# Performance work log

Hardware: AMD Instinct MI355X
Metric: run time of the kernel (lower is better)

Reference implementation:

```python
import jax, jax.numpy as jnp
import numpy as np

DIM = 1024
CTX_DIM = 768
H = 16


def setup_inputs() -> dict:
    key = jax.random.key(0)
    k1, k2, k3, k4, k5 = jax.random.split(key, 5)
    x = jax.random.normal(k1, (2, 2048, DIM), dtype=jnp.float32)
    context = jax.random.normal(k2, (2, 2048, CTX_DIM), dtype=jnp.float32)
    # Linear weights stored as [in, out] (y = x @ W); no biases per module.
    s = 0.02
    Wq = jax.random.normal(k3, (DIM, DIM), dtype=jnp.float32) * s
    Wkv = jax.random.normal(k4, (CTX_DIM, 2 * DIM), dtype=jnp.float32) * s
    Wo = jax.random.normal(k5, (DIM, DIM), dtype=jnp.float32) * s
    return {"x": x, "context": context, "Wq": Wq, "Wkv": Wkv, "Wo": Wo}


def reference(x, context, Wq, Wkv, Wo):
    B, N, C = x.shape
    Dh = C // H  # head dim
    scale = Dh ** -0.5
    M = context.shape[1]
    q = (x @ Wq).reshape(B, N, H, Dh).transpose(0, 2, 1, 3)      # [B,H,N,Dh]
    kv = context @ Wkv                                            # [B,M,2C]
    k, v = jnp.split(kv, 2, axis=-1)
    k = k.reshape(B, M, H, Dh).transpose(0, 2, 1, 3)              # [B,H,M,Dh]
    v = v.reshape(B, M, H, Dh).transpose(0, 2, 1, 3)              # [B,H,M,Dh]
    attn = jax.nn.softmax(jnp.einsum('bhnd,bhmd->bhnm', q, k) * scale, axis=-1)
    out = jnp.einsum('bhnm,bhmd->bhnd', attn, v)                  # [B,H,N,Dh]
    out = out.transpose(0, 2, 1, 3).reshape(B, N, C)
    return out @ Wo  # dropout is identity in eval / p=0
```

## Files before the change

### kernel.cpp

```cpp
#include <hip/hip_runtime.h>

typedef __attribute__((ext_vector_type(4))) float f32x4;
typedef __attribute__((ext_vector_type(8))) short short8;
typedef __attribute__((ext_vector_type(4))) unsigned int u32x4;
typedef unsigned short u16;
typedef unsigned int u32;
typedef unsigned long long u64;

__device__ __forceinline__ u16 f2bf(float f) {
  u32 u = __builtin_bit_cast(u32, f);
  u += 0x7fffu + ((u >> 16) & 1u);
  return (u16)(u >> 16);
}
__device__ __forceinline__ u16 f2bf_t(float f) {
  return (u16)(__builtin_bit_cast(u32, f) >> 16);
}

__device__ __forceinline__ void gl2lds16(const u16* g, const u16* l) {
  __builtin_amdgcn_global_load_lds(
      (const __attribute__((address_space(1))) u32*)g,
      (__attribute__((address_space(3))) u32*)(u32)(u64)l,
      16, 0, 0);
}

__device__ __forceinline__ void cast_body(const float* __restrict__ s,
                                          u16* __restrict__ d, int blk,
                                          int tid) {
  long i = (long)blk * 256 + tid;
  const f32x4* sp = (const f32x4*)(s + i * 8);
  f32x4 a = sp[0], b = sp[1];
  u16 t[8];
#pragma unroll
  for (int j = 0; j < 4; j++) {
    t[j] = f2bf(a[j]);
    t[4 + j] = f2bf(b[j]);
  }
  *(u32x4*)(d + i * 8) = *(u32x4*)t;
}

__device__ __forceinline__ void transpose_body(const float* __restrict__ W,
                                               u16* __restrict__ WT, int K,
                                               int N, int k0, int n0, int tid,
                                               u16* T) {
#pragma unroll
  for (int i = 0; i < 4; i++) {
    int c = tid + 256 * i;
    int row = c >> 4;
    int ch = c & 15;
    f32x4 f = *(const f32x4*)(W + (long)(k0 + row) * N + n0 + ch * 4);
#pragma unroll
    for (int j = 0; j < 4; j++) T[(ch * 4 + j) * 72 + row] = f2bf(f[j]);
  }
  __syncthreads();
#pragma unroll
  for (int i = 0; i < 2; i++) {
    int c = tid + 256 * i;
    int row = c >> 3;
    int ch = c & 7;
    u32x4 v = *(u32x4*)&T[row * 72 + ch * 8];
    *(u32x4*)(WT + (long)(n0 + row) * K + k0 + ch * 8) = v;
  }
}

__global__ __launch_bounds__(256) void prep(
    const float* __restrict__ x, const float* __restrict__ ctx,
    const float* __restrict__ Wq, const float* __restrict__ Wkv,
    const float* __restrict__ Wo, u16* __restrict__ xb,
    u16* __restrict__ ctxb, u16* __restrict__ wqT, u16* __restrict__ wkvT,
    u16* __restrict__ woT) {
  __shared__ __align__(16) u16 T[64 * 72];
  const int b = blockIdx.x, tid = threadIdx.x;
  if (b < 2048) {
    cast_body(x, xb, b, tid);
  } else if (b < 3584) {
    cast_body(ctx, ctxb, b - 2048, tid);
  } else if (b < 3840) {
    int idx = b - 3584;
    transpose_body(Wq, wqT, 1024, 1024, (idx >> 4) * 64, (idx & 15) * 64, tid, T);
  } else if (b < 4224) {
    int idx = b - 3840;
    transpose_body(Wkv, wkvT, 768, 2048, (idx >> 5) * 64, (idx & 31) * 64, tid, T);
  } else {
    int idx = b - 4224;
    transpose_body(Wo, woT, 1024, 1024, (idx >> 4) * 64, (idx & 15) * 64, tid, T);
  }
}

__device__ __forceinline__ void gemm128_core(
    const u16* __restrict__ A, const u16* __restrict__ Bt, int Kstride,
    int Klen, long brow, long bcol, int tid, u16* As, u16* Bs,
    f32x4 (&acc)[4][4]) {
  const int lane = tid & 63, wv = tid >> 6;
  const int l15 = lane & 15, quad = lane >> 4;
  const int wr = (wv >> 1) * 64, wc = (wv & 1) * 64;
  const int sr = lane >> 3, sc = lane & 7;
  const int csw = ((sc ^ sr) & 7) * 8;

  const u16* ag[4];
  const u16* bg[4];
  const u16* al[4];
  const u16* bl[4];
#pragma unroll
  for (int n = 0; n < 4; n++) {
    int row = wv * 32 + n * 8;
    ag[n] = A + (brow + row + sr) * (long)Kstride + csw;
    al[n] = &As[row * 64];
    bg[n] = Bt + (bcol + row + sr) * (long)Kstride + csw;
    bl[n] = &Bs[row * 64];
  }

  for (int kt = 0; kt < Klen; kt += 64) {
    __syncthreads();
#pragma unroll
    for (int n = 0; n < 4; n++) gl2lds16(ag[n] + kt, al[n]);
#pragma unroll
    for (int n = 0; n < 4; n++) gl2lds16(bg[n] + kt, bl[n]);
    __syncthreads();
#pragma unroll
    for (int kk = 0; kk < 2; kk++) {
      short8 af[4], bf[4];
#pragma unroll
      for (int i = 0; i < 4; i++) {
        int row = wr + i * 16 + l15;
        af[i] = *(short8*)&As[row * 64 + (((kk * 4 + quad) ^ (row & 7)) << 3)];
      }
#pragma unroll
      for (int j = 0; j < 4; j++) {
        int row = wc + j * 16 + l15;
        bf[j] = *(short8*)&Bs[row * 64 + (((kk * 4 + quad) ^ (row & 7)) << 3)];
      }
#pragma unroll
      for (int i = 0; i < 4; i++)
#pragma unroll
        for (int j = 0; j < 4; j++)
          acc[i][j] = __builtin_amdgcn_mfma_f32_16x16x32_bf16(
              af[i], bf[j], acc[i][j], 0, 0, 0);
    }
  }
}

__global__ __launch_bounds__(256, 3) void fused_qkv(
    const u16* __restrict__ xb, const u16* __restrict__ ctxb,
    const u16* __restrict__ wqT, const u16* __restrict__ wkvT,
    u16* __restrict__ Qb, u16* __restrict__ Kfrag, u16* __restrict__ Vfrag,
    float qscale) {
  __shared__ __align__(16) u16 As[128 * 64];
  __shared__ __align__(16) u16 Bs[128 * 64];
  const int tid = threadIdx.x;
  const int lane = tid & 63, wv = tid >> 6;
  const int l15 = lane & 15, quad = lane >> 4;
  const int wr = (wv >> 1) * 64, wc = (wv & 1) * 64;

  f32x4 acc[4][4];
#pragma unroll
  for (int i = 0; i < 4; i++)
#pragma unroll
    for (int j = 0; j < 4; j++) acc[i][j] = (f32x4){0.f, 0.f, 0.f, 0.f};

  int bid = blockIdx.x;
  if (bid < 256) {
    long brow = (long)(bid >> 3) * 128, bcol = (long)(bid & 7) * 128;
    gemm128_core(xb, wqT, 1024, 1024, brow, bcol, tid, As, Bs, acc);
#pragma unroll
    for (int i = 0; i < 4; i++)
#pragma unroll
      for (int j = 0; j < 4; j++)
#pragma unroll
        for (int r = 0; r < 4; r++) {
          long row = brow + wr + i * 16 + quad * 4 + r;
          long col = bcol + wc + j * 16 + l15;
          Qb[row * 1024 + col] = f2bf(acc[i][j][r] * qscale);
        }
    return;
  }

  bid -= 256;
  long brow = (long)(bid >> 4) * 128, bcol = (long)(bid & 15) * 128;
  gemm128_core(ctxb, wkvT, 768, 768, brow, bcol, tid, As, Bs, acc);

  const bool is_k = (bcol < 1024);
  __syncthreads();
#pragma unroll
  for (int round = 0; round < 2; round++) {
    if ((wv >> 1) == round) {
      if (is_k) {
#pragma unroll
        for (int i = 0; i < 4; i++)
#pragma unroll
          for (int j = 0; j < 4; j++) {
            int d = j * 16 + l15;
            int off = (wv & 1) * 4096 + ((d >> 5) * 4 + i) * 512 +
                      (((d >> 3) & 3) * 16 + quad * 4) * 8 + (d & 7);
#pragma unroll
            for (int r = 0; r < 4; r++) As[off + r * 8] = f2bf(acc[i][j][r]);
          }
      } else {
#pragma unroll
        for (int i = 0; i < 4; i++)
#pragma unroll
          for (int j = 0; j < 4; j++) {
            int off = (wv & 1) * 4096 + ((i >> 1) * 4 + j) * 512 +
                      (quad * 16 + l15) * 8 + (i & 1) * 4;
            u16 t4[4];
#pragma unroll
            for (int r = 0; r < 4; r++) t4[r] = f2bf(acc[i][j][r]);
            *(u64*)&As[off] = *(const u64*)t4;
          }
      }
    }
    __syncthreads();
    long mg = brow + round * 64;
    int b_ = (int)(mg >> 11), mt = (int)((mg >> 6) & 31);
#pragma unroll
    for (int h2 = 0; h2 < 2; h2++) {
      int h = (int)((is_k ? bcol : bcol - 1024) >> 6) + h2;
      u16* dst = (is_k ? Kfrag : Vfrag) + ((long)(b_ * 16 + h) * 32 + mt) * 4096;
#pragma unroll
      for (int p = 0; p < 2; p++) {
        int c = p * 256 + tid;
        *(u32x4*)(dst + c * 8) = *(u32x4*)&As[h2 * 4096 + c * 8];
      }
    }
    __syncthreads();
  }
}

__global__ __launch_bounds__(256, 3) void gemm_o(
    const u16* __restrict__ A, const u16* __restrict__ Bt,
    float* __restrict__ C) {
  __shared__ __align__(16) u16 As[128 * 64];
  __shared__ __align__(16) u16 Bs[128 * 64];
  const int tid = threadIdx.x;
  const int lane = tid & 63, wv = tid >> 6;
  const int l15 = lane & 15, quad = lane >> 4;
  const int wr = (wv >> 1) * 64, wc = (wv & 1) * 64;
  long brow = (long)blockIdx.y * 128, bcol = (long)blockIdx.x * 128;

  f32x4 acc[4][4];
#pragma unroll
  for (int i = 0; i < 4; i++)
#pragma unroll
    for (int j = 0; j < 4; j++) acc[i][j] = (f32x4){0.f, 0.f, 0.f, 0.f};

  gemm128_core(A, Bt, 1024, 1024, brow, bcol, tid, As, Bs, acc);

#pragma unroll
  for (int i = 0; i < 4; i++)
#pragma unroll
    for (int j = 0; j < 4; j++)
#pragma unroll
      for (int r = 0; r < 4; r++) {
        long row = brow + wr + i * 16 + quad * 4 + r;
        long col = bcol + wc + j * 16 + l15;
        C[row * 1024 + col] = acc[i][j][r];
      }
}

__global__ __launch_bounds__(256, 2) void attn_kernel(
    const u16* __restrict__ Q, const u16* __restrict__ Kfrag,
    const u16* __restrict__ Vfrag, u16* __restrict__ AO) {
  const int tid = threadIdx.x;
  const int lane = tid & 63, wave = tid >> 6;
  const int l15 = lane & 15, quad = lane >> 4;
  const int bh = blockIdx.y;
  const int b = bh >> 4, h = bh & 15;
  const long qrow0 = (long)b * 2048 + blockIdx.x * 128;

  short8 qf[2][2];
#pragma unroll
  for (int qt = 0; qt < 2; qt++)
#pragma unroll
    for (int kk = 0; kk < 2; kk++)
      qf[qt][kk] = *(const short8*)&Q[(qrow0 + wave * 32 + qt * 16 + l15) * 1024 +
                                      h * 64 + kk * 32 + quad * 8];

  f32x4 O[2][5];
#pragma unroll
  for (int qt = 0; qt < 2; qt++)
#pragma unroll
    for (int dt = 0; dt < 5; dt++) O[qt][dt] = (f32x4){0.f, 0.f, 0.f, 0.f};

  u32x4 ones_u = {0x3F803F80u, 0x3F803F80u, 0x3F803F80u, 0x3F803F80u};
  short8 ones = __builtin_bit_cast(short8, ones_u);

  const u16* kbase = Kfrag + (long)bh * 32 * 4096 + lane * 8;
  const u16* vbase = Vfrag + (long)bh * 32 * 4096 + lane * 8;

  auto load_k = [&](short8(&kf)[2][4], int tile) {
    const u16* kt = kbase + (long)tile * 4096;
#pragma unroll
    for (int kk = 0; kk < 2; kk++)
#pragma unroll
      for (int t = 0; t < 4; t++)
        kf[kk][t] = *(const short8*)(kt + (kk * 4 + t) * 512);
  };

  auto step = [&](short8(&kc)[2][4], short8(&kn)[2][4], int tile) {
    short8 vf[2][4];
    const u16* vt = vbase + (long)tile * 4096;
#pragma unroll
    for (int kk = 0; kk < 2; kk++)
#pragma unroll
      for (int dt = 0; dt < 4; dt++)
        vf[kk][dt] = *(const short8*)(vt + (kk * 4 + dt) * 512);
    if (tile + 1 < 32) load_k(kn, tile + 1);

    f32x4 s[4][2];
#pragma unroll
    for (int m4 = 0; m4 < 4; m4++)
#pragma unroll
      for (int qt = 0; qt < 2; qt++) s[m4][qt] = (f32x4){0.f, 0.f, 0.f, 0.f};
#pragma unroll
    for (int kk = 0; kk < 2; kk++)
#pragma unroll
      for (int m4 = 0; m4 < 4; m4++)
#pragma unroll
        for (int qt = 0; qt < 2; qt++)
          s[m4][qt] = __builtin_amdgcn_mfma_f32_16x16x32_bf16(
              kc[kk][m4], qf[qt][kk], s[m4][qt], 0, 0, 0);

#pragma unroll
    for (int kk = 0; kk < 2; kk++) {
#pragma unroll
      for (int qt = 0; qt < 2; qt++) {
        u32 w[4];
#pragma unroll
        for (int half = 0; half < 2; half++) {
          f32x4 sv = s[2 * kk + half][qt];
          u32 lo = (u32)f2bf_t(__builtin_amdgcn_exp2f(sv[0] - 24.f)) |
                   ((u32)f2bf_t(__builtin_amdgcn_exp2f(sv[1] - 24.f)) << 16);
          u32 hi = (u32)f2bf_t(__builtin_amdgcn_exp2f(sv[2] - 24.f)) |
                   ((u32)f2bf_t(__builtin_amdgcn_exp2f(sv[3] - 24.f)) << 16);
          w[half * 2] = lo;
          w[half * 2 + 1] = hi;
        }
        short8 pa = __builtin_bit_cast(short8, *(u32x4*)w);
#pragma unroll
        for (int dt = 0; dt < 4; dt++)
          O[qt][dt] = __builtin_amdgcn_mfma_f32_16x16x32_bf16(
              pa, vf[kk][dt], O[qt][dt], 0, 0, 0);
        O[qt][4] = __builtin_amdgcn_mfma_f32_16x16x32_bf16(
            pa, ones, O[qt][4], 0, 0, 0);
      }
    }
  };

  short8 ka[2][4], kb2[2][4];
  load_k(ka, 0);
  for (int tile = 0; tile < 32; tile += 2) {
    step(ka, kb2, tile);
    step(kb2, ka, tile + 1);
  }

#pragma unroll
  for (int qt = 0; qt < 2; qt++) {
    float inv[4];
#pragma unroll
    for (int r = 0; r < 4; r++) inv[r] = 1.f / O[qt][4][r];
#pragma unroll
    for (int dt = 0; dt < 4; dt++)
#pragma unroll
      for (int r = 0; r < 4; r++) {
        long row = qrow0 + wave * 32 + qt * 16 + quad * 4 + r;
        int col = h * 64 + dt * 16 + l15;
        AO[row * 1024 + col] = f2bf(O[qt][dt][r] * inv[r]);
      }
  }
}

extern "C" void kernel_launch(void* const* d_in, const int* in_sizes, int n_in,
                              void* d_out, int out_size, void* d_ws,
                              size_t ws_size, hipStream_t stream) {
  const float* x = (const float*)d_in[0];
  const float* ctx = (const float*)d_in[1];
  const float* Wq = (const float*)d_in[2];
  const float* Wkv = (const float*)d_in[3];
  const float* Wo = (const float*)d_in[4];
  float* out = (float*)d_out;

  u16* ws = (u16*)d_ws;
  u16* wqT = ws;
  u16* wkvT = wqT + 1048576;
  u16* woT = wkvT + 1572864;
  u16* Qb = woT + 1048576;
  u16* Kfrag = Qb + 4194304;
  u16* Vfrag = Kfrag + 4194304;
  u16* xb = Vfrag + 4194304;
  u16* ctxb = xb + 4194304;
  u16* AOb = xb;

  const float qscale = 0.125f * 1.4426950408889634f;

  prep<<<dim3(4480), 256, 0, stream>>>(x, ctx, Wq, Wkv, Wo, xb, ctxb, wqT,
                                       wkvT, woT);

  fused_qkv<<<dim3(768), 256, 0, stream>>>(xb, ctxb, wqT, wkvT, Qb, Kfrag,
                                           Vfrag, qscale);

  attn_kernel<<<dim3(16, 32), 256, 0, stream>>>(Qb, Kfrag, Vfrag, AOb);

  gemm_o<<<dim3(8, 32), 256, 0, stream>>>(AOb, woT, out);
}
```

Baseline: 191.2 us.

## Stage K/V tiles in LDS and split key range across two wave halves

The attention kernel now uses 512 threads per block. K/V fragments are staged into double-buffered shared memory with global_load_lds, so the four query-chunk waves share one copy instead of each wave reading them from global memory separately. The key sequence is split between two groups of four waves, and their partial outputs and row sums are combined through LDS at the end. This reduces global K/V traffic and register pressure, at the cost of block-wide barriers every tile and a final reduction step.

```diff
diff --git a/kernel.cpp b/kernel.cpp
--- a/kernel.cpp
+++ b/kernel.cpp
@@ -256,22 +256,24 @@
       }
 }
 
-__global__ __launch_bounds__(256, 2) void attn_kernel(
+__global__ __launch_bounds__(512, 4) void attn_kernel(
     const u16* __restrict__ Q, const u16* __restrict__ Kfrag,
     const u16* __restrict__ Vfrag, u16* __restrict__ AO) {
+  __shared__ __align__(16) u16 smem[2][4][4096];
   const int tid = threadIdx.x;
-  const int lane = tid & 63, wave = tid >> 6;
+  const int lane = tid & 63, wv = tid >> 6;
+  const int qc = wv & 3, half = wv >> 2;
   const int l15 = lane & 15, quad = lane >> 4;
   const int bh = blockIdx.y;
   const int b = bh >> 4, h = bh & 15;
-  const long qrow0 = (long)b * 2048 + blockIdx.x * 128;
+  const long qrow0 = (long)b * 2048 + blockIdx.x * 128 + qc * 32;
 
   short8 qf[2][2];
 #pragma unroll
   for (int qt = 0; qt < 2; qt++)
 #pragma unroll
     for (int kk = 0; kk < 2; kk++)
-      qf[qt][kk] = *(const short8*)&Q[(qrow0 + wave * 32 + qt * 16 + l15) * 1024 +
+      qf[qt][kk] = *(const short8*)&Q[(qrow0 + qt * 16 + l15) * 1024 +
                                       h * 64 + kk * 32 + quad * 8];
 
   f32x4 O[2][5];
@@ -283,88 +285,109 @@
   u32x4 ones_u = {0x3F803F80u, 0x3F803F80u, 0x3F803F80u, 0x3F803F80u};
   short8 ones = __builtin_bit_cast(short8, ones_u);
 
-  const u16* kbase = Kfrag + (long)bh * 32 * 4096 + lane * 8;
-  const u16* vbase = Vfrag + (long)bh * 32 * 4096 + lane * 8;
-
-  auto load_k = [&](short8(&kf)[2][4], int tile) {
-    const u16* kt = kbase + (long)tile * 4096;
-#pragma unroll
-    for (int kk = 0; kk < 2; kk++)
+  const u16* kg0 = Kfrag + (long)bh * 32 * 4096;
+  const u16* vg0 = Vfrag + (long)bh * 32 * 4096;
+  const int so = wv * 512 + lane * 8;
+
+  auto stage = [&](int nb, int i) {
+    const u16* k0 = kg0 + (long)i * 4096 + so;
+    const u16* v0 = vg0 + (long)i * 4096 + so;
+    gl2lds16(k0, &smem[nb][0][wv * 512]);
+    gl2lds16(v0, &smem[nb][1][wv * 512]);
+    gl2lds16(k0 + 16 * 4096, &smem[nb][2][wv * 512]);
+    gl2lds16(v0 + 16 * 4096, &smem[nb][3][wv * 512]);
+  };
+
+  stage(0, 0);
+  __syncthreads();
+
+  for (int i = 0; i < 16; i++) {
+    const int cur = i & 1;
+    if (i < 15) stage(cur ^ 1, i + 1);
+
+    const u16* Ks = &smem[cur][half * 2][0] + lane * 8;
+    const u16* Vs = &smem[cur][half * 2 + 1][0] + lane * 8;
+
+    f32x4 s[4][2];
+#pragma unroll
+    for (int m4 = 0; m4 < 4; m4++)
+#pragma unroll
+      for (int qt = 0; qt < 2; qt++) s[m4][qt] = (f32x4){0.f, 0.f, 0.f, 0.f};
+#pragma unroll
+    for (int kk = 0; kk < 2; kk++) {
+      short8 kf[4];
 #pragma unroll
       for (int t = 0; t < 4; t++)
-        kf[kk][t] = *(const short8*)(kt + (kk * 4 + t) * 512);
-  };
-
-  auto step = [&](short8(&kc)[2][4], short8(&kn)[2][4], int tile) {
-    short8 vf[2][4];
-    const u16* vt = vbase + (long)tile * 4096;
-#pragma unroll
-    for (int kk = 0; kk < 2; kk++)
-#pragma unroll
-      for (int dt = 0; dt < 4; dt++)
-        vf[kk][dt] = *(const short8*)(vt + (kk * 4 + dt) * 512);
-    if (tile + 1 < 32) load_k(kn, tile + 1);
-
-    f32x4 s[4][2];
-#pragma unroll
-    for (int m4 = 0; m4 < 4; m4++)
-#pragma unroll
-      for (int qt = 0; qt < 2; qt++) s[m4][qt] = (f32x4){0.f, 0.f, 0.f, 0.f};
-#pragma unroll
-    for (int kk = 0; kk < 2; kk++)
+        kf[t] = *(const short8*)(Ks + (kk * 4 + t) * 512);
 #pragma unroll
       for (int m4 = 0; m4 < 4; m4++)
 #pragma unroll
         for (int qt = 0; qt < 2; qt++)
           s[m4][qt] = __builtin_amdgcn_mfma_f32_16x16x32_bf16(
-              kc[kk][m4], qf[qt][kk], s[m4][qt], 0, 0, 0);
+              kf[m4], qf[qt][kk], s[m4][qt], 0, 0, 0);
+    }
 
 #pragma unroll
     for (int kk = 0; kk < 2; kk++) {
+      short8 vf[4];
+#pragma unroll
+      for (int dt = 0; dt < 4; dt++)
+        vf[dt] = *(const short8*)(Vs + (kk * 4 + dt) * 512);
 #pragma unroll
       for (int qt = 0; qt < 2; qt++) {
         u32 w[4];
 #pragma unroll
-        for (int half = 0; half < 2; half++) {
-          f32x4 sv = s[2 * kk + half][qt];
+        for (int hw = 0; hw < 2; hw++) {
+          f32x4 sv = s[2 * kk + hw][qt];
           u32 lo = (u32)f2bf_t(__builtin_amdgcn_exp2f(sv[0] - 24.f)) |
                    ((u32)f2bf_t(__builtin_amdgcn_exp2f(sv[1] - 24.f)) << 16);
           u32 hi = (u32)f2bf_t(__builtin_amdgcn_exp2f(sv[2] - 24.f)) |
                    ((u32)f2bf_t(__builtin_amdgcn_exp2f(sv[3] - 24.f)) << 16);
-          w[half * 2] = lo;
-          w[half * 2 + 1] = hi;
+          w[hw * 2] = lo;
+          w[hw * 2 + 1] = hi;
         }
         short8 pa = __builtin_bit_cast(short8, *(u32x4*)w);
 #pragma unroll
         for (int dt = 0; dt < 4; dt++)
           O[qt][dt] = __builtin_amdgcn_mfma_f32_16x16x32_bf16(
-              pa, vf[kk][dt], O[qt][dt], 0, 0, 0);
+              pa, vf[dt], O[qt][dt], 0, 0, 0);
         O[qt][4] = __builtin_amdgcn_mfma_f32_16x16x32_bf16(
             pa, ones, O[qt][4], 0, 0, 0);
       }
     }
-  };
-
-  short8 ka[2][4], kb2[2][4];
-  load_k(ka, 0);
-  for (int tile = 0; tile < 32; tile += 2) {
-    step(ka, kb2, tile);
-    step(kb2, ka, tile + 1);
-  }
-
-#pragma unroll
-  for (int qt = 0; qt < 2; qt++) {
-    float inv[4];
-#pragma unroll
-    for (int r = 0; r < 4; r++) inv[r] = 1.f / O[qt][4][r];
-#pragma unroll
-    for (int dt = 0; dt < 4; dt++)
-#pragma unroll
-      for (int r = 0; r < 4; r++) {
-        long row = qrow0 + wave * 32 + qt * 16 + quad * 4 + r;
-        int col = h * 64 + dt * 16 + l15;
-        AO[row * 1024 + col] = f2bf(O[qt][dt][r] * inv[r]);
-      }
+    __syncthreads();
+  }
+
+  f32x4* cb = (f32x4*)&smem[0][0][0];
+  if (half) {
+#pragma unroll
+    for (int qt = 0; qt < 2; qt++)
+#pragma unroll
+      for (int dt = 0; dt < 5; dt++)
+        cb[(qc * 64 + lane) * 10 + qt * 5 + dt] = O[qt][dt];
+  }
+  __syncthreads();
+  if (!half) {
+#pragma unroll
+    for (int qt = 0; qt < 2; qt++)
+#pragma unroll
+      for (int dt = 0; dt < 5; dt++)
+        O[qt][dt] += cb[(qc * 64 + lane) * 10 + qt * 5 + dt];
+
+#pragma unroll
+    for (int qt = 0; qt < 2; qt++) {
+      float inv[4];
+#pragma unroll
+      for (int r = 0; r < 4; r++) inv[r] = 1.f / O[qt][4][r];
+#pragma unroll
+      for (int dt = 0; dt < 4; dt++)
+#pragma unroll
+        for (int r = 0; r < 4; r++) {
+          long row = qrow0 + qt * 16 + quad * 4 + r;
+          int col = h * 64 + dt * 16 + l15;
+          AO[row * 1024 + col] = f2bf(O[qt][dt][r] * inv[r]);
+        }
+    }
   }
 }
 
@@ -397,7 +420,7 @@
   fused_qkv<<<dim3(768), 256, 0, stream>>>(xb, ctxb, wqT, wkvT, Qb, Kfrag,
                                            Vfrag, qscale);
 
-  attn_kernel<<<dim3(16, 32), 256, 0, stream>>>(Qb, Kfrag, Vfrag, AOb);
+  attn_kernel<<<dim3(16, 32), 512, 0, stream>>>(Qb, Kfrag, Vfrag, AOb);
 
   gemm_o<<<dim3(8, 32), 256, 0, stream>>>(AOb, woT, out);
 }
```

Measured after the change: 178.1 us. 1.07x faster.
